# Kernel tuning notes

Measured on AMD Instinct MI355X. Metric: run time of the kernel, lower is better.

## Reference

```python
import jax, jax.numpy as jnp
import numpy as np

HEAD_SIZE = 128
D_MODEL = 1024


def setup_inputs() -> dict:
    key = jax.random.key(0)
    kx, kq, kk, kv = jax.random.split(key, 4)
    B, T, C = 8, 2048, D_MODEL
    scale = 1.0 / np.sqrt(C)
    x = jax.random.normal(kx, (B, T, C), dtype=jnp.float32)
    # Dense(head_size, use_bias=False) weights, shape [C, head_size]
    Wq = jax.random.normal(kq, (C, HEAD_SIZE), dtype=jnp.float32) * scale
    Wk = jax.random.normal(kk, (C, HEAD_SIZE), dtype=jnp.float32) * scale
    Wv = jax.random.normal(kv, (C, HEAD_SIZE), dtype=jnp.float32) * scale
    return {"x": x, "Wq": Wq, "Wk": Wk, "Wv": Wv}


def reference(x, Wq, Wk, Wv):
    B, T, C = x.shape
    q = jnp.einsum('btc,ch->bth', x, Wq)  # [B,T,H]
    k = jnp.einsum('btc,ch->bth', x, Wk)
    v = jnp.einsum('btc,ch->bth', x, Wv)
    # NOTE: original scales by C**-0.5 (input channels), not head_size**-0.5
    scale = jnp.asarray(C, x.dtype) ** -0.5
    wei = jnp.einsum('bqh,bkh->bqk', q, k) * scale  # [B,T,T]
    causal = jnp.tril(jnp.ones((T, T), dtype=bool))
    wei = jnp.where(causal, wei, -jnp.inf)
    wei = jax.nn.softmax(wei, axis=-1)
    # dropout is identity in inference mode
    out = jnp.einsum('bqk,bkh->bqh', wei, v)  # [B,T,H]
    return out
```

## Files before the change

### kernel.cpp

```cpp
#include <hip/hip_runtime.h>

#define HS 128
#define DM 1024
#define BB 8
#define TT 2048

typedef __bf16 bf16;
typedef __bf16 bf16x8 __attribute__((ext_vector_type(8)));
typedef float f32x4 __attribute__((ext_vector_type(4)));

#define MFMA16(a, b, c) __builtin_amdgcn_mfma_f32_16x16x32_bf16(a, b, c, 0, 0, 0)
#define RAW_BARRIER() asm volatile("s_barrier" ::: "memory")

__device__ __forceinline__ void gll16(const bf16* g, bf16* l) {
  __builtin_amdgcn_global_load_lds(
      (const __attribute__((address_space(1))) void*)g,
      (__attribute__((address_space(3))) void*)l, 16, 0, 0);
}

__global__ __launch_bounds__(256) void wt_kernel(const float* __restrict__ Wq,
                                                 const float* __restrict__ Wk,
                                                 const float* __restrict__ Wv,
                                                 bf16* __restrict__ Wt) {
  __shared__ bf16 lt[128][72];
  const int mat = blockIdx.y;
  const float* W = mat == 0 ? Wq : (mat == 1 ? Wk : Wv);
  const int k0 = blockIdx.x * 64;
  const int t = threadIdx.x;
  for (int i = 0; i < 32; ++i) {
    int idx = t + i * 256;
    int k = idx >> 7;
    int h = idx & 127;
    lt[h][k] = (bf16)W[(size_t)(k0 + k) * HS + h];
  }
  __syncthreads();
  int h = t >> 1, half = t & 1;
  const uint4* src = (const uint4*)&lt[h][half * 32];
  uint4* dst = (uint4*)(Wt + ((size_t)mat * 128 + h) * DM + k0 + half * 32);
  dst[0] = src[0]; dst[1] = src[1]; dst[2] = src[2]; dst[3] = src[3];
}

__global__ __launch_bounds__(256, 3) void qkv_kernel(const float* __restrict__ x,
                                                     const bf16* __restrict__ Wt,
                                                     bf16* __restrict__ Q,
                                                     bf16* __restrict__ K,
                                                     bf16* __restrict__ Vt) {
  __shared__ __align__(16) char qsm[32768];
  bf16 (*wsb)[8192] = (bf16(*)[8192])qsm;
  bf16* vts = (bf16*)qsm;
  const int t = threadIdx.x, w = t >> 6, lane = t & 63, rl = lane & 15, quad = lane >> 4;
  const int g = blockIdx.x;
  const int wgid = (g & 7) * 96 + (g >> 3);
  const int rt = wgid / 3, nb = wgid - rt * 3;
  const int row0 = rt * 64;
  const int rw = w & 1, cw = w >> 1;
  f32x4 acc[2][4] = {};
  float4 xr[8];
  bf16x8 af[4];

  auto stage = [&](int kt, int bufi) {
#pragma unroll
    for (int i2 = 0; i2 < 4; ++i2) {
      int s = w * 4 + i2;
      int row = s * 8 + (lane >> 3);
      int cg = (lane & 7) ^ (row & 7);
      gll16(Wt + (size_t)(nb * 128 + row) * DM + kt * 64 + cg * 8, &wsb[bufi][s * 512]);
    }
  };
  auto loadx = [&](int kt) {
#pragma unroll
    for (int kc = 0; kc < 2; ++kc)
#pragma unroll
      for (int rf = 0; rf < 2; ++rf) {
        int idx = kc * 2 + rf;
        int ar = rw * 32 + rf * 16 + rl;
        const float* p = x + (size_t)(row0 + ar) * DM + kt * 64 + kc * 32 + quad * 8;
        xr[idx * 2] = *(const float4*)p;
        xr[idx * 2 + 1] = *(const float4*)(p + 4);
      }
  };

  loadx(0);
  stage(0, 0);
  stage(1, 1);
  for (int kt = 0; kt < 16; ++kt) {
    const int cur = kt & 1;
    if (kt < 15) asm volatile("s_waitcnt vmcnt(4)" ::: "memory");
    else         asm volatile("s_waitcnt vmcnt(0)" ::: "memory");
    RAW_BARRIER();
#pragma unroll
    for (int j = 0; j < 4; ++j) {
      float4 f0 = xr[j * 2], f1 = xr[j * 2 + 1];
      bf16x8 tv;
      tv[0] = (bf16)f0.x; tv[1] = (bf16)f0.y; tv[2] = (bf16)f0.z; tv[3] = (bf16)f0.w;
      tv[4] = (bf16)f1.x; tv[5] = (bf16)f1.y; tv[6] = (bf16)f1.z; tv[7] = (bf16)f1.w;
      af[j] = tv;
    }
    if (kt < 15) loadx(kt + 1);
#pragma unroll
    for (int kc = 0; kc < 2; ++kc)
#pragma unroll
      for (int cf = 0; cf < 4; ++cf) {
        int br = cw * 64 + cf * 16 + rl;
        int cb = kc * 4 + quad;
        bf16x8 bb = *(const bf16x8*)&wsb[cur][br * 64 + ((cb ^ (br & 7)) << 3)];
        acc[0][cf] = MFMA16(af[kc * 2 + 0], bb, acc[0][cf]);
        acc[1][cf] = MFMA16(af[kc * 2 + 1], bb, acc[1][cf]);
      }
    RAW_BARRIER();
    if (kt < 14) stage(kt + 2, cur);
  }
  if (nb < 2) {
    bf16* dst = nb == 0 ? Q : K;
#pragma unroll
    for (int cf = 0; cf < 4; ++cf) {
      int hcol = cw * 64 + cf * 16 + rl;
#pragma unroll
      for (int rf = 0; rf < 2; ++rf)
#pragma unroll
        for (int r = 0; r < 4; ++r) {
          int tg = row0 + rw * 32 + rf * 16 + quad * 4 + r;
          dst[((size_t)tg << 7) + hcol] = (bf16)acc[rf][cf][r];
        }
    }
  } else {
#pragma unroll
    for (int cf = 0; cf < 4; ++cf) {
      int hcol = cw * 64 + cf * 16 + rl;
#pragma unroll
      for (int rf = 0; rf < 2; ++rf)
#pragma unroll
        for (int r = 0; r < 4; ++r) {
          int trow = rw * 32 + rf * 16 + quad * 4 + r;
          vts[hcol * 72 + trow] = (bf16)acc[rf][cf][r];
        }
    }
    __syncthreads();
    const int h = t >> 1, half = t & 1;
    const bf16* src = vts + h * 72 + half * 32;
    bf16* dst = Vt + ((size_t)((row0 >> 11) * 128 + h) << 11) + (row0 & 2047) + half * 32;
#pragma unroll
    for (int j = 0; j < 4; ++j)
      ((bf16x8*)dst)[j] = ((const bf16x8*)src)[j];
  }
}

__global__ __launch_bounds__(256) void attn_kernel(const bf16* __restrict__ Qb,
                                                   const bf16* __restrict__ Kb,
                                                   const bf16* __restrict__ Vtb,
                                                   float* __restrict__ out) {
  __shared__ __align__(16) char smem[79104];
  bf16* qs = (bf16*)smem;
  bf16* ks = (bf16*)(smem + 8192);
  bf16* vt = (bf16*)(smem + 40960);
  float* Of = (float*)smem;
  float* ml = (float*)(smem + 78848);
  const int t = threadIdx.x, w = t >> 6, lane = t & 63, rl = lane & 15, quad = lane >> 4;
  const int wrow = w >> 1, kh = w & 1;
  const int rank = blockIdx.x >> 3, b = blockIdx.x & 7;
  const int qi = 63 - rank;
  const int q0 = qi * 32;
  const size_t base = (size_t)b * TT;
  const int KT = (qi >> 1) + 1;

#pragma unroll
  for (int i2 = 0; i2 < 2; ++i2) {
    int s = w * 2 + i2;
    int row = s * 4 + (lane >> 4);
    int ch = (lane & 15) ^ (row & 15);
    gll16(Qb + ((base + q0 + row) << 7) + ch * 8, qs + s * 512);
  }
  auto stageKV = [&](int slot) {
    int kt = min(slot, KT - 1);
    int bufi = slot & 1;
    bf16* ksb = ks + bufi * 8192;
    bf16* vtb = vt + bufi * 8192;
#pragma unroll
    for (int i2 = 0; i2 < 4; ++i2) {
      int s = w * 4 + i2;
      int rowk = s * 4 + (lane >> 4);
      int chk = (lane & 15) ^ (rowk & 15);
      gll16(Kb + ((base + kt * 64 + rowk) << 7) + chk * 8, ksb + s * 512);
      int rowv = s * 8 + (lane >> 3);
      int chv = (lane & 7) ^ (rowv & 7);
      gll16(Vtb + ((size_t)(b * 128 + rowv) << 11) + kt * 64 + chv * 8, vtb + s * 512);
    }
  };
  stageKV(0);
  stageKV(1);

  f32x4 o[8] = {};
  float lrow[4] = {0.f, 0.f, 0.f, 0.f};
  bf16x8 aq[4];
  bf16* psw = (bf16*)(smem + 73728) + w * 640;

  for (int i = 0; i < KT; ++i) {
    const int cur = i & 1;
    asm volatile("s_waitcnt vmcnt(8)" ::: "memory");
    RAW_BARRIER();
    if (i == 0) {
      const int arow = wrow * 16 + rl;
#pragma unroll
      for (int hc = 0; hc < 4; ++hc)
        aq[hc] = *(const bf16x8*)(qs + arow * 128 + ((((hc << 2) + quad) ^ (arow & 15)) << 3));
    }
    bf16* ksb = ks + cur * 8192;
    bf16* vtb = vt + cur * 8192;
    f32x4 s4[2] = {};
#pragma unroll
    for (int hc = 0; hc < 4; ++hc) {
#pragma unroll
      for (int c = 0; c < 2; ++c) {
        int brow = (kh * 2 + c) * 16 + rl;
        bf16x8 bb = *(const bf16x8*)(ksb + brow * 128 + ((((hc << 2) + quad) ^ (brow & 15)) << 3));
        s4[c] = MFMA16(aq[hc], bb, s4[c]);
      }
    }
    const bool diag = (i == KT - 1);
#pragma unroll
    for (int r = 0; r < 4; ++r) {
      int rloc = quad * 4 + r;
      int rowg = q0 + wrow * 16 + rloc;
      float psum = 0.f;
#pragma unroll
      for (int c = 0; c < 2; ++c) {
        int colg = i * 64 + kh * 32 + c * 16 + rl;
        float p = (diag && colg > rowg) ? 0.f : __expf(s4[c][r] * 0.03125f - 6.0f);
        psum += p;
        psw[rloc * 40 + c * 16 + rl] = (bf16)p;
      }
      lrow[r] += psum;
    }
    bf16x8 pa = *(const bf16x8*)(psw + rl * 40 + quad * 8);
#pragma unroll
    for (int ht = 0; ht < 8; ++ht) {
      int brow = ht * 16 + rl;
      bf16x8 bb = *(const bf16x8*)(vtb + brow * 64 + ((((kh << 2) + quad) ^ (brow & 7)) << 3));
      o[ht] = MFMA16(pa, bb, o[ht]);
    }
    RAW_BARRIER();
    if (i + 2 <= KT) stageKV(i + 2);
  }

#pragma unroll
  for (int r = 0; r < 4; ++r)
#pragma unroll
    for (int off = 1; off < 16; off <<= 1) lrow[r] += __shfl_xor(lrow[r], off, 64);
  __syncthreads();
#pragma unroll
  for (int ht = 0; ht < 8; ++ht)
#pragma unroll
    for (int r = 0; r < 4; ++r)
      Of[kh * 4096 + (wrow * 16 + quad * 4 + r) * 128 + ht * 16 + rl] = o[ht][r];
  if (rl == 0)
#pragma unroll
    for (int r = 0; r < 4; ++r) ml[kh * 32 + wrow * 16 + quad * 4 + r] = lrow[r];
  __syncthreads();
#pragma unroll
  for (int r = 0; r < 4; ++r) {
    int rowl = wrow * 16 + quad * 4 + r;
    float inv = 1.f / (ml[rowl] + ml[32 + rowl]);
#pragma unroll
    for (int hh = 0; hh < 4; ++hh) {
      int col = kh * 64 + hh * 16 + rl;
      out[((base + q0 + rowl) << 7) + col] =
          (Of[rowl * 128 + col] + Of[4096 + rowl * 128 + col]) * inv;
    }
  }
}

extern "C" void kernel_launch(void* const* d_in, const int* in_sizes, int n_in,
                              void* d_out, int out_size, void* d_ws, size_t ws_size,
                              hipStream_t stream) {
  const float* x = (const float*)d_in[0];
  const float* Wq = (const float*)d_in[1];
  const float* Wk = (const float*)d_in[2];
  const float* Wv = (const float*)d_in[3];
  float* out = (float*)d_out;
  char* ws = (char*)d_ws;
  bf16* Wt = (bf16*)ws;
  bf16* Q = (bf16*)(ws + 786432);
  bf16* K = (bf16*)(ws + 786432 + 4194304);
  bf16* Vt = (bf16*)(ws + 786432 + 2 * 4194304);
  wt_kernel<<<dim3(16, 3), 256, 0, stream>>>(Wq, Wk, Wv, Wt);
  qkv_kernel<<<dim3(768), 256, 0, stream>>>(x, Wt, Q, K, Vt);
  attn_kernel<<<dim3(512), 256, 0, stream>>>(Q, K, Vt, out);
}
```

Measured before the change: 185.1 us.

## Stage x tiles into LDS via async loads and reorder attention block schedule

The QKV projection kernel now streams fp32 x tiles directly into LDS with global_load_lds, double-buffered alongside the weight tiles. This replaces per-thread register loads of x, and the K step is halved to 32 with a new swizzled layout. The launch-bounds occupancy hint is removed. The attention kernel's block-to-query-tile mapping changes so the first 32 ranks take the longest tiles and the rest take the shortest ones ascending, which changes load balancing across workgroups.

```diff
diff --git a/kernel.cpp b/kernel.cpp
--- a/kernel.cpp
+++ b/kernel.cpp
@@ -13,6 +13,11 @@
 #define RAW_BARRIER() asm volatile("s_barrier" ::: "memory")
 
 __device__ __forceinline__ void gll16(const bf16* g, bf16* l) {
+  __builtin_amdgcn_global_load_lds(
+      (const __attribute__((address_space(1))) void*)g,
+      (__attribute__((address_space(3))) void*)l, 16, 0, 0);
+}
+__device__ __forceinline__ void gll16f(const float* g, float* l) {
   __builtin_amdgcn_global_load_lds(
       (const __attribute__((address_space(1))) void*)g,
       (__attribute__((address_space(3))) void*)l, 16, 0, 0);
@@ -40,13 +45,14 @@
   dst[0] = src[0]; dst[1] = src[1]; dst[2] = src[2]; dst[3] = src[3];
 }
 
-__global__ __launch_bounds__(256, 3) void qkv_kernel(const float* __restrict__ x,
-                                                     const bf16* __restrict__ Wt,
-                                                     bf16* __restrict__ Q,
-                                                     bf16* __restrict__ K,
-                                                     bf16* __restrict__ Vt) {
+__global__ __launch_bounds__(256) void qkv_kernel(const float* __restrict__ x,
+                                                  const bf16* __restrict__ Wt,
+                                                  bf16* __restrict__ Q,
+                                                  bf16* __restrict__ K,
+                                                  bf16* __restrict__ Vt) {
   __shared__ __align__(16) char qsm[32768];
-  bf16 (*wsb)[8192] = (bf16(*)[8192])qsm;
+  float* xsf = (float*)qsm;
+  bf16* wsb = (bf16*)(qsm + 16384);
   bf16* vts = (bf16*)qsm;
   const int t = threadIdx.x, w = t >> 6, lane = t & 63, rl = lane & 15, quad = lane >> 4;
   const int g = blockIdx.x;
@@ -54,61 +60,59 @@
   const int rt = wgid / 3, nb = wgid - rt * 3;
   const int row0 = rt * 64;
   const int rw = w & 1, cw = w >> 1;
+  const int l3 = lane >> 3, l7 = lane & 7, e = l7 ^ l3;
   f32x4 acc[2][4] = {};
-  float4 xr[8];
-  bf16x8 af[4];
 
   auto stage = [&](int kt, int bufi) {
 #pragma unroll
-    for (int i2 = 0; i2 < 4; ++i2) {
-      int s = w * 4 + i2;
-      int row = s * 8 + (lane >> 3);
-      int cg = (lane & 7) ^ (row & 7);
-      gll16(Wt + (size_t)(nb * 128 + row) * DM + kt * 64 + cg * 8, &wsb[bufi][s * 512]);
+    for (int i2 = 0; i2 < 2; ++i2) {
+      int s = w * 2 + i2;
+      int row = s * 8 + l3;
+      gll16f(x + (size_t)(row0 + row) * DM + kt * 32 + e * 4,
+             xsf + bufi * 2048 + s * 256);
+    }
+#pragma unroll
+    for (int i2 = 0; i2 < 2; ++i2) {
+      int s = w * 2 + i2;
+      int L = s * 8 + l3;
+      int r = 2 * L + (e & 1);
+      gll16(Wt + (size_t)(nb * 128 + r) * DM + kt * 32 + (e >> 1) * 8,
+            wsb + bufi * 4096 + s * 512);
     }
   };
-  auto loadx = [&](int kt) {
-#pragma unroll
-    for (int kc = 0; kc < 2; ++kc)
-#pragma unroll
-      for (int rf = 0; rf < 2; ++rf) {
-        int idx = kc * 2 + rf;
-        int ar = rw * 32 + rf * 16 + rl;
-        const float* p = x + (size_t)(row0 + ar) * DM + kt * 64 + kc * 32 + quad * 8;
-        xr[idx * 2] = *(const float4*)p;
-        xr[idx * 2 + 1] = *(const float4*)(p + 4);
-      }
-  };
-
-  loadx(0);
+
   stage(0, 0);
   stage(1, 1);
-  for (int kt = 0; kt < 16; ++kt) {
+  for (int kt = 0; kt < 32; ++kt) {
     const int cur = kt & 1;
-    if (kt < 15) asm volatile("s_waitcnt vmcnt(4)" ::: "memory");
+    if (kt < 31) asm volatile("s_waitcnt vmcnt(4)" ::: "memory");
     else         asm volatile("s_waitcnt vmcnt(0)" ::: "memory");
     RAW_BARRIER();
-#pragma unroll
-    for (int j = 0; j < 4; ++j) {
-      float4 f0 = xr[j * 2], f1 = xr[j * 2 + 1];
+    const float* xc = xsf + cur * 2048;
+    const bf16* wc = wsb + cur * 4096;
+    bf16x8 a[2];
+#pragma unroll
+    for (int rf = 0; rf < 2; ++rf) {
+      int ar = rw * 32 + rf * 16 + rl;
+      int c0 = quad * 2;
+      float4 f0 = *(const float4*)&xc[ar * 32 + (((c0) ^ (ar & 7)) << 2)];
+      float4 f1 = *(const float4*)&xc[ar * 32 + (((c0 + 1) ^ (ar & 7)) << 2)];
       bf16x8 tv;
       tv[0] = (bf16)f0.x; tv[1] = (bf16)f0.y; tv[2] = (bf16)f0.z; tv[3] = (bf16)f0.w;
       tv[4] = (bf16)f1.x; tv[5] = (bf16)f1.y; tv[6] = (bf16)f1.z; tv[7] = (bf16)f1.w;
-      af[j] = tv;
-    }
-    if (kt < 15) loadx(kt + 1);
-#pragma unroll
-    for (int kc = 0; kc < 2; ++kc)
-#pragma unroll
-      for (int cf = 0; cf < 4; ++cf) {
-        int br = cw * 64 + cf * 16 + rl;
-        int cb = kc * 4 + quad;
-        bf16x8 bb = *(const bf16x8*)&wsb[cur][br * 64 + ((cb ^ (br & 7)) << 3)];
-        acc[0][cf] = MFMA16(af[kc * 2 + 0], bb, acc[0][cf]);
-        acc[1][cf] = MFMA16(af[kc * 2 + 1], bb, acc[1][cf]);
-      }
-    RAW_BARRIER();
-    if (kt < 14) stage(kt + 2, cur);
+      a[rf] = tv;
+    }
+#pragma unroll
+    for (int cf = 0; cf < 4; ++cf) {
+      int br = cw * 64 + cf * 16 + rl;
+      int L = br >> 1;
+      int up = ((quad << 1) | (br & 1)) ^ (L & 7);
+      bf16x8 bb = *(const bf16x8*)&wc[L * 64 + (up << 3)];
+      acc[0][cf] = MFMA16(a[0], bb, acc[0][cf]);
+      acc[1][cf] = MFMA16(a[1], bb, acc[1][cf]);
+    }
+    RAW_BARRIER();
+    if (kt < 30) stage(kt + 2, cur);
   }
   if (nb < 2) {
     bf16* dst = nb == 0 ? Q : K;
@@ -124,6 +128,7 @@
         }
     }
   } else {
+    __syncthreads();
 #pragma unroll
     for (int cf = 0; cf < 4; ++cf) {
       int hcol = cw * 64 + cf * 16 + rl;
@@ -158,7 +163,7 @@
   const int t = threadIdx.x, w = t >> 6, lane = t & 63, rl = lane & 15, quad = lane >> 4;
   const int wrow = w >> 1, kh = w & 1;
   const int rank = blockIdx.x >> 3, b = blockIdx.x & 7;
-  const int qi = 63 - rank;
+  const int qi = (rank < 32) ? (63 - rank) : (rank - 32);
   const int q0 = qi * 32;
   const size_t base = (size_t)b * TT;
   const int KT = (qi >> 1) + 1;
```

Measured after the change: 161.9 us. 12.6% less time.
